# Performance work log

Measured on AMD Instinct MI355X. Metric: run time of the kernel, lower is better.

## Reference

```python
import jax, jax.numpy as jnp
import numpy as np

IN_F = 1024
OUT_F = 1024
B, S = 8, 4096


def _pack_ternary(tern):
    # encoding: -1 -> 0, 0 -> 1, +1 -> 2; 4 values per byte, matching torch pack_ternary_weights
    enc = (tern + 1.0).astype(jnp.int32).reshape(-1)  # length divisible by 4 here
    return (enc[0::4] | (enc[1::4] << 2) | (enc[2::4] << 4) | (enc[3::4] << 6)).astype(jnp.int32)


def setup_inputs() -> dict:
    key = jax.random.key(0)
    kx, kw = jax.random.split(key)
    x = jax.random.normal(kx, (B, S, IN_F), dtype=jnp.float32)
    w = jax.random.normal(kw, (OUT_F, IN_F), dtype=jnp.float32) * 0.02
    # quantize_weights_158bit
    scale = jnp.maximum(jnp.mean(jnp.abs(w)), 1e-5)
    wn = w / scale
    tern = jnp.sign(wn) * (jnp.abs(wn) > 0.5).astype(jnp.float32)
    packed = _pack_ternary(tern)
    bias = jnp.zeros((OUT_F,), dtype=jnp.float32)
    return {"x": x, "packed_weight": packed, "weight_scale": scale.reshape(1), "bias": bias}


def reference(x, packed_weight, weight_scale, bias):
    n = OUT_F * IN_F
    shifts = jnp.array([0, 2, 4, 6], dtype=jnp.int32)
    # Faithful to original unpack_ternary_weights: concatenate bit-planes, then truncate.
    # (This is a permutation of the packed order, replicated deliberately.)
    enc = ((packed_weight[None, :] >> shifts[:, None]) & 3).reshape(-1)[:n]
    w = (enc.astype(jnp.float32) - 1.0).reshape(OUT_F, IN_F) * weight_scale  # dequant ternary
    # training path: INT8 per-token activation fake-quant
    act_scale = 127.0 / jnp.maximum(jnp.max(jnp.abs(x), axis=-1, keepdims=True), 1e-5)
    x_dq = jnp.clip(jnp.round(x * act_scale), -128.0, 127.0) / act_scale
    return jnp.einsum('bsi,oi->bso', x_dq, w) + bias
```

## Files before the change

kernel.cpp:

```cpp
#include <hip/hip_runtime.h>
#include <hip/hip_bf16.h>
#include <stdint.h>

typedef int i32x4 __attribute__((ext_vector_type(4)));

constexpr int IN_F = 1024;
constexpr int OUT_F = 1024;
constexpr int M_TOT = 8 * 4096;
constexpr int K_TOT = IN_F;
constexpr int N_TOT = OUT_F;

__global__ __launch_bounds__(256) void quant_kernel(
    const float* __restrict__ x,
    const float* __restrict__ wscale,
    int8_t* __restrict__ q,
    float* __restrict__ inv_row)
{
    const int row = blockIdx.x;
    const int t = threadIdx.x;
    const float4 v = reinterpret_cast<const float4*>(x + (size_t)row * IN_F)[t];
    float m = fmaxf(fmaxf(fabsf(v.x), fabsf(v.y)), fmaxf(fabsf(v.z), fabsf(v.w)));
    #pragma unroll
    for (int off = 32; off > 0; off >>= 1)
        m = fmaxf(m, __shfl_xor(m, off));
    __shared__ float smax[4];
    if ((t & 63) == 0) smax[t >> 6] = m;
    __syncthreads();
    m = fmaxf(fmaxf(smax[0], smax[1]), fmaxf(smax[2], smax[3]));
    const float a = fmaxf(m, 1e-5f);
    const float as = 127.0f / a;

    char4 o;
    o.x = (char)(int)fminf(fmaxf(rintf(v.x * as), -128.0f), 127.0f);
    o.y = (char)(int)fminf(fmaxf(rintf(v.y * as), -128.0f), 127.0f);
    o.z = (char)(int)fminf(fmaxf(rintf(v.z * as), -128.0f), 127.0f);
    o.w = (char)(int)fminf(fmaxf(rintf(v.w * as), -128.0f), 127.0f);
    reinterpret_cast<char4*>(q + (size_t)row * IN_F)[t] = o;
    if (t == 0) inv_row[row] = (a / 127.0f) * wscale[0];
}

__global__ __launch_bounds__(256) void unpack_kernel(
    const int* __restrict__ packed,
    int8_t* __restrict__ wt)
{
    const int o = blockIdx.x;
    const int k0 = threadIdx.x * 4;
    const int sh = (o >> 8) * 2;
    const int pbase = ((o & 255) << 10) + k0;
    const int4 pw = *reinterpret_cast<const int4*>(packed + pbase);
    char4 r;
    r.x = (char)(((pw.x >> sh) & 3) - 1);
    r.y = (char)(((pw.y >> sh) & 3) - 1);
    r.z = (char)(((pw.z >> sh) & 3) - 1);
    r.w = (char)(((pw.w >> sh) & 3) - 1);
    *reinterpret_cast<char4*>(wt + (size_t)o * IN_F + k0) = r;
}

constexpr int BM = 256, BN = 256, BK = 128;
constexpr int NT = K_TOT / BK;

__global__ __launch_bounds__(512, 2) void gemm_kernel(
    const int8_t* __restrict__ qa,
    const int8_t* __restrict__ wb,
    const float* __restrict__ inv_row,
    const float* __restrict__ bias,
    float* __restrict__ out)
{
    int bid = blockIdx.x;
    bid = (bid & 7) * ((int)gridDim.x >> 3) + (bid >> 3);
    const int tm = bid >> 2;
    const int tn = bid & 3;

    const int tid = threadIdx.x;
    const int lane = tid & 63;
    const int wid = tid >> 6;
    const int wr = wid >> 2;
    const int wc = wid & 3;

    __shared__ int8_t lds[2][2][2][128 * 128];

    const int rowA0 = tm * BM;
    const int rowB0 = tn * BN;
    const int frow = lane & 15;
    const int fq = lane >> 4;

    i32x4 acc[8][4] = {};

    auto stage = [&](int buf, int ab, int region, int kt) {
        const int8_t* base = ab ? wb : qa;
        #pragma unroll
        for (int j = 0; j < 2; ++j) {
            const int c = j * 512 + tid;
            const int rl = c >> 3, cc = c & 7;
            const int grow = ab ? (rowB0 + region * 128 + rl)
                                : (rowA0 + (rl & 64) * 2 + region * 64 + (rl & 63));
            const int scc = cc ^ (rl & 7);
            const int8_t* src = base + (size_t)grow * K_TOT + kt * BK + scc * 16;
            __builtin_amdgcn_global_load_lds(
                (const __attribute__((address_space(1))) void*)src,
                (__attribute__((address_space(3))) void*)&lds[buf][ab][region][c * 16],
                16, 0, 0);
        }
    };

    auto ldA = [&](int buf, int region, int mf, int ks) -> i32x4 {
        const int local = wr * 64 + (mf & 3) * 16 + frow;
        const int ch = (ks * 4 + fq) ^ (local & 7);
        return *reinterpret_cast<const i32x4*>(&lds[buf][0][region][local * 128 + ch * 16]);
    };
    auto ldB = [&](int buf, int nf, int ks) -> i32x4 {
        const int region = wc >> 1;
        const int local = (wc & 1) * 64 + nf * 16 + frow;
        const int ch = (ks * 4 + fq) ^ (local & 7);
        return *reinterpret_cast<const i32x4*>(&lds[buf][1][region][local * 128 + ch * 16]);
    };

    stage(0, 1, 0, 0); stage(0, 1, 1, 0); stage(0, 0, 0, 0); stage(0, 0, 1, 0);
    asm volatile("s_waitcnt vmcnt(0)" ::: "memory");
    __builtin_amdgcn_s_barrier();

    for (int T = 0; T < NT; ++T) {
        const int cur = T & 1, nxt = cur ^ 1;
        const bool st = (T + 1 < NT);
        i32x4 aF[4][2], bF[4][2];

        #pragma unroll
        for (int mf = 0; mf < 4; ++mf)
            #pragma unroll
            for (int ks = 0; ks < 2; ++ks)
                aF[mf][ks] = ldA(cur, 0, mf, ks);
        #pragma unroll
        for (int nf = 0; nf < 4; ++nf)
            #pragma unroll
            for (int ks = 0; ks < 2; ++ks)
                bF[nf][ks] = ldB(cur, nf, ks);
        if (st) { stage(nxt, 1, 0, T + 1); stage(nxt, 1, 1, T + 1); }
        __builtin_amdgcn_s_barrier();
        asm volatile("s_waitcnt lgkmcnt(0)" ::: "memory");
        __builtin_amdgcn_sched_barrier(0);
        __builtin_amdgcn_s_setprio(1);
        #pragma unroll
        for (int mf = 0; mf < 4; ++mf)
            #pragma unroll
            for (int nf = 0; nf < 4; ++nf)
                #pragma unroll
                for (int ks = 0; ks < 2; ++ks)
                    acc[mf][nf] = __builtin_amdgcn_mfma_i32_16x16x64_i8(
                        aF[mf][ks], bF[nf][ks], acc[mf][nf], 0, 0, 0);
        __builtin_amdgcn_s_setprio(0);
        if (st) asm volatile("s_waitcnt vmcnt(4)" ::: "memory");
        else    asm volatile("s_waitcnt vmcnt(0)" ::: "memory");
        __builtin_amdgcn_s_barrier();

        #pragma unroll
        for (int mf = 0; mf < 4; ++mf)
            #pragma unroll
            for (int ks = 0; ks < 2; ++ks)
                aF[mf][ks] = ldA(cur, 1, mf, ks);
        if (st) { stage(nxt, 0, 0, T + 1); stage(nxt, 0, 1, T + 1); }
        __builtin_amdgcn_s_barrier();
        asm volatile("s_waitcnt lgkmcnt(0)" ::: "memory");
        __builtin_amdgcn_sched_barrier(0);
        __builtin_amdgcn_s_setprio(1);
        #pragma unroll
        for (int mf = 0; mf < 4; ++mf)
            #pragma unroll
            for (int nf = 0; nf < 4; ++nf)
                #pragma unroll
                for (int ks = 0; ks < 2; ++ks)
                    acc[4 + mf][nf] = __builtin_amdgcn_mfma_i32_16x16x64_i8(
                        aF[mf][ks], bF[nf][ks], acc[4 + mf][nf], 0, 0, 0);
        __builtin_amdgcn_s_setprio(0);
        asm volatile("s_waitcnt vmcnt(2)" ::: "memory");
        __builtin_amdgcn_s_barrier();
    }

    #pragma unroll
    for (int mi = 0; mi < 8; ++mi) {
        #pragma unroll
        for (int j = 0; j < 4; ++j) {
            const int gm = rowA0 + wr * 128 + mi * 16 + fq * 4 + j;
            const float sc = inv_row[gm];
            #pragma unroll
            for (int nf = 0; nf < 4; ++nf) {
                const int gn = rowB0 + wc * 64 + nf * 16 + frow;
                out[(size_t)gm * N_TOT + gn] = (float)acc[mi][nf][j] * sc + bias[gn];
            }
        }
    }
}

extern "C" void kernel_launch(void* const* d_in, const int* in_sizes, int n_in,
                              void* d_out, int out_size, void* d_ws, size_t ws_size,
                              hipStream_t stream) {
    const float* x = (const float*)d_in[0];
    const int* packed = (const int*)d_in[1];
    const float* wscale = (const float*)d_in[2];
    const float* bias = (const float*)d_in[3];
    float* out = (float*)d_out;

    int8_t* q = (int8_t*)d_ws;
    int8_t* wt = (int8_t*)((char*)d_ws + (size_t)M_TOT * K_TOT);
    float* inv_row = (float*)((char*)d_ws + (size_t)M_TOT * K_TOT + (size_t)N_TOT * K_TOT);

    quant_kernel<<<M_TOT, 256, 0, stream>>>(x, wscale, q, inv_row);
    unpack_kernel<<<OUT_F, 256, 0, stream>>>(packed, wt);
    gemm_kernel<<<(M_TOT / BM) * (N_TOT / BN), 512, 0, stream>>>(q, wt, inv_row, bias, out);
}
```

Before: 86.79 us.

## Fuse activation quantization into GEMM with cross-block counter synchronization

```diff
diff --git a/kernel.cpp b/kernel.cpp
--- a/kernel.cpp
+++ b/kernel.cpp
@@ -7,37 +7,8 @@
 constexpr int IN_F = 1024;
 constexpr int OUT_F = 1024;
 constexpr int M_TOT = 8 * 4096;
-constexpr int K_TOT = IN_F;
-constexpr int N_TOT = OUT_F;
-
-__global__ __launch_bounds__(256) void quant_kernel(
-    const float* __restrict__ x,
-    const float* __restrict__ wscale,
-    int8_t* __restrict__ q,
-    float* __restrict__ inv_row)
-{
-    const int row = blockIdx.x;
-    const int t = threadIdx.x;
-    const float4 v = reinterpret_cast<const float4*>(x + (size_t)row * IN_F)[t];
-    float m = fmaxf(fmaxf(fabsf(v.x), fabsf(v.y)), fmaxf(fabsf(v.z), fabsf(v.w)));
-    #pragma unroll
-    for (int off = 32; off > 0; off >>= 1)
-        m = fmaxf(m, __shfl_xor(m, off));
-    __shared__ float smax[4];
-    if ((t & 63) == 0) smax[t >> 6] = m;
-    __syncthreads();
-    m = fmaxf(fmaxf(smax[0], smax[1]), fmaxf(smax[2], smax[3]));
-    const float a = fmaxf(m, 1e-5f);
-    const float as = 127.0f / a;
-
-    char4 o;
-    o.x = (char)(int)fminf(fmaxf(rintf(v.x * as), -128.0f), 127.0f);
-    o.y = (char)(int)fminf(fmaxf(rintf(v.y * as), -128.0f), 127.0f);
-    o.z = (char)(int)fminf(fmaxf(rintf(v.z * as), -128.0f), 127.0f);
-    o.w = (char)(int)fminf(fmaxf(rintf(v.w * as), -128.0f), 127.0f);
-    reinterpret_cast<char4*>(q + (size_t)row * IN_F)[t] = o;
-    if (t == 0) inv_row[row] = (a / 127.0f) * wscale[0];
-}
+constexpr int K_TOT = 1024;
+constexpr int N_TOT = 1024;
 
 __global__ __launch_bounds__(256) void unpack_kernel(
     const int* __restrict__ packed,
@@ -59,11 +30,14 @@
 constexpr int BM = 256, BN = 256, BK = 128;
 constexpr int NT = K_TOT / BK;
 
-__global__ __launch_bounds__(512, 2) void gemm_kernel(
-    const int8_t* __restrict__ qa,
+__global__ __launch_bounds__(512, 2) void fused_kernel(
+    const float* __restrict__ x,
     const int8_t* __restrict__ wb,
-    const float* __restrict__ inv_row,
+    const float* __restrict__ wscale,
     const float* __restrict__ bias,
+    int8_t* __restrict__ q,
+    float* __restrict__ inv_row,
+    int* __restrict__ cnt,
     float* __restrict__ out)
 {
     int bid = blockIdx.x;
@@ -78,6 +52,67 @@
     const int wc = wid & 3;
 
     __shared__ int8_t lds[2][2][2][128 * 128];
+    __shared__ int sready;
+
+    const float wsc = wscale[0];
+    const int c8 = lane & 7;
+    auto quant_rows = [&](int rows0) {
+        const int r = rows0 + wid * 8 + (lane >> 3);
+        const float4* xr = reinterpret_cast<const float4*>(x + (size_t)r * IN_F);
+        float m = 0.f;
+        #pragma unroll
+        for (int j = 0; j < 8; ++j) {
+            #pragma unroll
+            for (int u = 0; u < 4; ++u) {
+                const float4 v = xr[4 * c8 + 32 * j + u];
+                m = fmaxf(m, fmaxf(fmaxf(fabsf(v.x), fabsf(v.y)),
+                                   fmaxf(fabsf(v.z), fabsf(v.w))));
+            }
+        }
+        m = fmaxf(m, __shfl_xor(m, 1));
+        m = fmaxf(m, __shfl_xor(m, 2));
+        m = fmaxf(m, __shfl_xor(m, 4));
+        const float a = fmaxf(m, 1e-5f);
+        const float as = 127.0f / a;
+        if (c8 == 0) inv_row[r] = (a / 127.0f) * wsc;
+        #pragma unroll
+        for (int j = 0; j < 8; ++j) {
+            int4 o4;
+            int* op = &o4.x;
+            #pragma unroll
+            for (int u = 0; u < 4; ++u) {
+                const float4 v = xr[4 * c8 + 32 * j + u];
+                const int b0 = (int)fminf(fmaxf(rintf(v.x * as), -128.f), 127.f) & 255;
+                const int b1 = (int)fminf(fmaxf(rintf(v.y * as), -128.f), 127.f) & 255;
+                const int b2 = (int)fminf(fmaxf(rintf(v.z * as), -128.f), 127.f) & 255;
+                const int b3 = (int)fminf(fmaxf(rintf(v.w * as), -128.f), 127.f) & 255;
+                op[u] = b0 | (b1 << 8) | (b2 << 16) | (b3 << 24);
+            }
+            reinterpret_cast<int4*>(q + (size_t)r * K_TOT)[c8 + 8 * j] = o4;
+        }
+    };
+
+    quant_rows(tm * 256 + tn * 64);
+    __threadfence();
+    __syncthreads();
+    if (tid == 0) {
+        atomicAdd(cnt + tm, 1);
+        int it = 0;
+        while (atomicAdd(cnt + tm, 0) < 4 && it < 20000) {
+            __builtin_amdgcn_s_sleep(8);
+            ++it;
+        }
+        sready = (it < 20000) ? 1 : 0;
+    }
+    __syncthreads();
+    if (!sready) {
+        #pragma unroll 1
+        for (int t2 = 1; t2 < 4; ++t2)
+            quant_rows(tm * 256 + ((tn + t2) & 3) * 64);
+        __threadfence();
+    }
+    __syncthreads();
+    __threadfence();
 
     const int rowA0 = tm * BM;
     const int rowB0 = tn * BN;
@@ -87,7 +122,7 @@
     i32x4 acc[8][4] = {};
 
     auto stage = [&](int buf, int ab, int region, int kt) {
-        const int8_t* base = ab ? wb : qa;
+        const int8_t* base = ab ? wb : q;
         #pragma unroll
         for (int j = 0; j < 2; ++j) {
             const int c = j * 512 + tid;
@@ -184,7 +219,9 @@
             #pragma unroll
             for (int nf = 0; nf < 4; ++nf) {
                 const int gn = rowB0 + wc * 64 + nf * 16 + frow;
-                out[(size_t)gm * N_TOT + gn] = (float)acc[mi][nf][j] * sc + bias[gn];
+                __builtin_nontemporal_store(
+                    (float)acc[mi][nf][j] * sc + bias[gn],
+                    &out[(size_t)gm * N_TOT + gn]);
             }
         }
     }
@@ -202,8 +239,11 @@
     int8_t* q = (int8_t*)d_ws;
     int8_t* wt = (int8_t*)((char*)d_ws + (size_t)M_TOT * K_TOT);
     float* inv_row = (float*)((char*)d_ws + (size_t)M_TOT * K_TOT + (size_t)N_TOT * K_TOT);
-
-    quant_kernel<<<M_TOT, 256, 0, stream>>>(x, wscale, q, inv_row);
+    int* cnt = (int*)((char*)d_ws + (size_t)M_TOT * K_TOT + (size_t)N_TOT * K_TOT
+                      + (size_t)M_TOT * sizeof(float));
+
+    hipMemsetAsync(cnt, 0, 128 * sizeof(int), stream);
     unpack_kernel<<<OUT_F, 256, 0, stream>>>(packed, wt);
-    gemm_kernel<<<(M_TOT / BM) * (N_TOT / BN), 512, 0, stream>>>(q, wt, inv_row, bias, out);
+    fused_kernel<<<(M_TOT / BM) * (N_TOT / BN), 512, 0, stream>>>(
+        x, wt, wscale, bias, q, inv_row, cnt, out);
 }
```

Result: slower. 311.2 us (+258.5%).
